# Optimization experiments

Hardware: AMD Instinct MI355X
Metric: run time of the kernel (lower is better)

## Reference

```python
import jax, jax.numpy as jnp
import numpy as np

N_NODES = 50000
N_EDGES = 1600000
IN_DIM = 128
HID = 128
SHARED = 64
N_GRAPHS = 2048


def setup_inputs() -> dict:
    key = jax.random.key(0)
    ks = jax.random.split(key, 16)
    x = jax.random.normal(ks[0], (N_NODES, IN_DIM), dtype=jnp.float32)
    edge_index = jax.random.randint(ks[1], (2, N_EDGES), 0, N_NODES, dtype=jnp.int64)
    batch = jnp.sort(jax.random.randint(ks[2], (N_NODES,), 0, N_GRAPHS, dtype=jnp.int64))

    def lin(k, fan_in, fan_out):
        bound = 1.0 / np.sqrt(fan_in)
        kw, kb = jax.random.split(k)
        W = jax.random.uniform(kw, (fan_in, fan_out), minval=-bound, maxval=bound, dtype=jnp.float32)
        b = jax.random.uniform(kb, (fan_out,), minval=-bound, maxval=bound, dtype=jnp.float32)
        return W, b

    W1a, b1a = lin(ks[3], IN_DIM, HID)
    W1b, b1b = lin(ks[4], HID, HID)
    W2a, b2a = lin(ks[5], HID, HID)
    W2b, b2b = lin(ks[6], HID, HID)
    Ws, bs = lin(ks[7], HID, SHARED)
    WlS, blS = lin(ks[8], SHARED, 1)
    WlP, blP = lin(ks[9], SHARED, 1)
    WnR, bnR = lin(ks[10], SHARED, 1)
    return dict(x=x, edge_index=edge_index, batch=batch,
                W1a=W1a, b1a=b1a, W1b=W1b, b1b=b1b,
                W2a=W2a, b2a=b2a, W2b=W2b, b2b=b2b,
                Ws=Ws, bs=bs, WlS=WlS, blS=blS, WlP=WlP, blP=blP, WnR=WnR, bnR=bnR)


def gin_conv(x, src, dst, Wa, ba, Wb, bb):
    # GINConv (eps=0): h_i = MLP(x_i + sum_{j->i} x_j)
    agg = jax.ops.segment_sum(x[src], dst, num_segments=N_NODES)
    h = x + agg
    h = jax.nn.relu(h @ Wa + ba)
    return h @ Wb + bb


def reference(x, edge_index, batch, W1a, b1a, W1b, b1b, W2a, b2a, W2b, b2b,
              Ws, bs, WlS, blS, WlP, blP, WnR, bnR):
    src, dst = edge_index[0], edge_index[1]
    h = jax.nn.relu(gin_conv(x, src, dst, W1a, b1a, W1b, b1b))
    h = jax.nn.relu(gin_conv(h, src, dst, W2a, b2a, W2b, b2b))
    # global mean pool over graph ids
    sums = jax.ops.segment_sum(h, batch, num_segments=N_GRAPHS)
    counts = jax.ops.segment_sum(jnp.ones((h.shape[0],), h.dtype), batch, num_segments=N_GRAPHS)
    pooled = sums / jnp.maximum(counts, 1.0)[:, None]
    g = jax.nn.relu(pooled @ Ws + bs)
    out_logS = (g @ WlS + blS)[:, 0]
    out_logP = (g @ WlP + blP)[:, 0]
    out_NR = (g @ WnR + bnR)[:, 0]
    return (out_logS, out_logP, out_NR)
```

## Files before the change

### kernel.cpp

```cpp
#include <hip/hip_runtime.h>
#include <hip/hip_bf16.h>


#define IN_DIM 128
#define NFINE 128
#define BIN_EPB 4096
#define SRCCH 8

typedef float  f32x4  __attribute__((ext_vector_type(4)));
typedef short  bf16x4 __attribute__((ext_vector_type(4)));
typedef short  bf16x8 __attribute__((ext_vector_type(8)));

__device__ __forceinline__ unsigned short bf16_rne(float v) {
    unsigned u = __float_as_uint(v);
    unsigned t = u + 0x7fffu + ((u >> 16) & 1u);
    return (unsigned short)(t >> 16);
}


__global__ __launch_bounds__(256) void f32_to_bf16_kernel(
    const float4* __restrict__ in, uint4* __restrict__ out, int n8)
{
    int i = blockIdx.x * 256 + threadIdx.x;
    if (i >= n8) return;
    float4 a = in[i * 2];
    float4 b = in[i * 2 + 1];
    float v[8] = {a.x, a.y, a.z, a.w, b.x, b.y, b.z, b.w};
    unsigned r[4];
#pragma unroll
    for (int j = 0; j < 4; ++j)
        r[j] = (unsigned)bf16_rne(v[j * 2]) | ((unsigned)bf16_rne(v[j * 2 + 1]) << 16);
    out[i] = make_uint4(r[0], r[1], r[2], r[3]);
}


__global__ __launch_bounds__(256) void conv_weights_kernel(
    const float* __restrict__ W0, const float* __restrict__ W1,
    const float* __restrict__ W2, const float* __restrict__ W3,
    unsigned short* __restrict__ Wh, unsigned short* __restrict__ Wl)
{
    int m   = blockIdx.x >> 6;
    int idx = (blockIdx.x & 63) * 256 + threadIdx.x;
    const float* W = (m == 0) ? W0 : (m == 1) ? W1 : (m == 2) ? W2 : W3;
    int k = idx >> 7, n = idx & 127;
    float v = W[idx];
    unsigned short hh = bf16_rne(v);
    float hf = __uint_as_float(((unsigned)hh) << 16);
    unsigned short ll = bf16_rne(v - hf);
    Wh[m * 16384 + n * 128 + k] = hh;
    Wl[m * 16384 + n * 128 + k] = ll;
}


__global__ __launch_bounds__(256) void bin_kernel(
    const int* __restrict__ src, const int* __restrict__ dst,
    int2* __restrict__ buckets, int* __restrict__ bcur,
    int n_edges, int n_nodes, int cap)
{
    __shared__ int cnt[NFINE];
    __shared__ int base[NFINE];
    for (int i = threadIdx.x; i < NFINE; i += 256) cnt[i] = 0;
    __syncthreads();

    const int e0 = blockIdx.x * BIN_EPB + threadIdx.x * 16;
    int ne = n_edges - e0;
    if (ne < 0) ne = 0;
    if (ne > 16) ne = 16;

    int d[16], s[16], off[16];
    if (ne == 16) {
#pragma unroll
        for (int q = 0; q < 4; ++q) {
            int4 dv = *(const int4*)(dst + e0 + q * 4);
            int4 sv = *(const int4*)(src + e0 + q * 4);
            d[q * 4 + 0] = dv.x; d[q * 4 + 1] = dv.y;
            d[q * 4 + 2] = dv.z; d[q * 4 + 3] = dv.w;
            s[q * 4 + 0] = sv.x; s[q * 4 + 1] = sv.y;
            s[q * 4 + 2] = sv.z; s[q * 4 + 3] = sv.w;
        }
    } else {
#pragma unroll
        for (int j = 0; j < 16; ++j) {
            d[j] = (j < ne) ? dst[e0 + j] : 0;
            s[j] = (j < ne) ? src[e0 + j] : 0;
        }
    }
#pragma unroll
    for (int j = 0; j < 16; ++j)
        if (j < ne) {
            int b = (int)(((long long)d[j] * NFINE) / n_nodes);
            off[j] = atomicAdd(&cnt[b], 1);
        }
    __syncthreads();
    for (int i = threadIdx.x; i < NFINE; i += 256)
        base[i] = atomicAdd(&bcur[i], cnt[i]);
    __syncthreads();
#pragma unroll
    for (int j = 0; j < 16; ++j)
        if (j < ne) {
            int b = (int)(((long long)d[j] * NFINE) / n_nodes);
            buckets[(size_t)b * cap + base[b] + off[j]] = make_int2(d[j], s[j]);
        }
}

__global__ __launch_bounds__(512) void csr_fused_kernel(
    const int2* __restrict__ buckets, const int* __restrict__ bcnt,
    int* __restrict__ row_start, int* __restrict__ csr_src,
    int cap, int n_nodes, int n_edges)
{
    __shared__ int bc[NFINE];
    __shared__ int h[4096];
    __shared__ int tsum[512];
    __shared__ int bbase_s;

    const int b = blockIdx.x;
    const int t = threadIdx.x;
    const int lo_n = (int)(((long long)b * n_nodes + NFINE - 1) / NFINE);
    const int hi_n = (int)(((long long)(b + 1) * n_nodes + NFINE - 1) / NFINE);
    const int sl = hi_n - lo_n;

    if (t < NFINE) bc[t] = bcnt[t];
#pragma unroll
    for (int j = 0; j < 8; ++j) h[t * 8 + j] = 0;
    __syncthreads();
    if (t == 0) {
        int s = 0;
        for (int i = 0; i < b; ++i) s += bc[i];
        bbase_s = s;
    }
    const int nb = bc[b];
    const int2* bp = buckets + (size_t)b * cap;
    __syncthreads();

    for (int i = t; i < nb; i += 512) {
        int2 e = bp[i];
        int key = (e.x - lo_n) * SRCCH + (int)(((long long)e.y * SRCCH) / n_nodes);
        atomicAdd(&h[key], 1);
    }
    __syncthreads();

    int base = 0;
#pragma unroll
    for (int j = 0; j < 8; ++j) {
        int v = h[t * 8 + j];
        h[t * 8 + j] = base;
        base += v;
    }
    tsum[t] = base;
    __syncthreads();
    int incl = tsum[t];
    for (int off = 1; off < 512; off <<= 1) {
        int tmp = (t >= off) ? tsum[t - off] : 0;
        __syncthreads();
        tsum[t] += tmp;
        __syncthreads();
        incl = tsum[t];
    }
    int texcl = incl - base + bbase_s;
#pragma unroll
    for (int j = 0; j < 8; ++j) h[t * 8 + j] += texcl;
    if (t < sl) row_start[lo_n + t] = h[t * SRCCH];
    if (b == NFINE - 1 && t == 0) row_start[n_nodes] = n_edges;
    __syncthreads();

    for (int i = t; i < nb; i += 512) {
        int2 e = bp[i];
        int key = (e.x - lo_n) * SRCCH + (int)(((long long)e.y * SRCCH) / n_nodes);
        csr_src[atomicAdd(&h[key], 1)] = e.y;
    }
}


__device__ __forceinline__ void add_row8(float acc[8], uint4 r) {
    union { unsigned u; float f; } c;
    c.u = r.x << 16;         acc[0] += c.f;
    c.u = r.x & 0xffff0000u; acc[1] += c.f;
    c.u = r.y << 16;         acc[2] += c.f;
    c.u = r.y & 0xffff0000u; acc[3] += c.f;
    c.u = r.z << 16;         acc[4] += c.f;
    c.u = r.z & 0xffff0000u; acc[5] += c.f;
    c.u = r.w << 16;         acc[6] += c.f;
    c.u = r.w & 0xffff0000u; acc[7] += c.f;
}

__global__ __launch_bounds__(256) void gather_agg_bf16_kernel(
    const float* __restrict__ xf,
    const uint4* __restrict__ xb,
    const int* __restrict__ row_start, const int* __restrict__ csr_src,
    float* __restrict__ out, int n_nodes)
{
    int t = blockIdx.x * 256 + threadIdx.x;
    int node = t >> 4;
    int lane = t & 15;
    if (node >= n_nodes) return;
    int lo = row_start[node];
    int hi = row_start[node + 1];

    const f32x4* xfr = (const f32x4*)(xf + (size_t)node * IN_DIM + lane * 8);
    f32x4 a0 = __builtin_nontemporal_load(xfr);
    f32x4 a1 = __builtin_nontemporal_load(xfr + 1);
    float acc[8] = {a0.x, a0.y, a0.z, a0.w, a1.x, a1.y, a1.z, a1.w};

    int e = lo;
    for (; e + 3 < hi; e += 4) {
        int s0 = csr_src[e];
        int s1 = csr_src[e + 1];
        int s2 = csr_src[e + 2];
        int s3 = csr_src[e + 3];
        uint4 r0 = xb[(size_t)s0 * 16 + lane];
        uint4 r1 = xb[(size_t)s1 * 16 + lane];
        uint4 r2 = xb[(size_t)s2 * 16 + lane];
        uint4 r3 = xb[(size_t)s3 * 16 + lane];
        add_row8(acc, r0);
        add_row8(acc, r1);
        add_row8(acc, r2);
        add_row8(acc, r3);
    }
    for (; e < hi; ++e) {
        uint4 r = xb[(size_t)csr_src[e] * 16 + lane];
        add_row8(acc, r);
    }

    f32x4 o0 = {acc[0], acc[1], acc[2], acc[3]};
    f32x4 o1 = {acc[4], acc[5], acc[6], acc[7]};
    f32x4* op = (f32x4*)(out + (size_t)node * IN_DIM + lane * 8);
    __builtin_nontemporal_store(o0, op);
    __builtin_nontemporal_store(o1, op + 1);
}

#define HSTRIDE 132

template <bool EMIT_BF16>
__global__ __launch_bounds__(128) void fused_mlp_kernel(
    const float* __restrict__ A,
    const unsigned short* __restrict__ Wa_h, const unsigned short* __restrict__ Wa_l,
    const float* __restrict__ ba,
    const unsigned short* __restrict__ Wb_h, const unsigned short* __restrict__ Wb_l,
    const float* __restrict__ bb,
    float* __restrict__ C, unsigned short* __restrict__ Cb, int M)
{
    __shared__ __align__(16) unsigned short Hh[64][HSTRIDE];
    __shared__ __align__(16) unsigned short Hl[64][HSTRIDE];

    const int t    = threadIdx.x;
    const int wave = t >> 6;
    const int lane = t & 63;
    const int l15  = lane & 15;
    const int quad = lane >> 4;
    const int wrow0 = wave * 32;
    const int row0  = blockIdx.x * 64 + wrow0;

    f32x4 acc[2][8];
#pragma unroll
    for (int ti = 0; ti < 2; ++ti)
#pragma unroll
        for (int ct = 0; ct < 8; ++ct) acc[ti][ct] = {0.f, 0.f, 0.f, 0.f};

    {
        int ar0 = row0 + l15;
        int ar1 = row0 + 16 + l15;
        const float* ap0 = A + (size_t)((ar0 < M) ? ar0 : (M - 1)) * IN_DIM + quad * 8;
        const float* ap1 = A + (size_t)((ar1 < M) ? ar1 : (M - 1)) * IN_DIM + quad * 8;
#pragma unroll
        for (int k0 = 0; k0 < IN_DIM; k0 += 32) {
            bf16x8 ah[2], al[2];
#pragma unroll
            for (int ti = 0; ti < 2; ++ti) {
                const float* ap = ti ? ap1 : ap0;
                f32x4 v0 = *(const f32x4*)(ap + k0);
                f32x4 v1 = *(const f32x4*)(ap + k0 + 4);
                float v[8] = {v0.x, v0.y, v0.z, v0.w, v1.x, v1.y, v1.z, v1.w};
                unsigned short h[8], l[8];
#pragma unroll
                for (int j = 0; j < 8; ++j) {
                    unsigned short hh = bf16_rne(v[j]);
                    h[j] = hh;
                    l[j] = bf16_rne(v[j] - __uint_as_float(((unsigned)hh) << 16));
                }
                ah[ti] = *(const bf16x8*)h;
                al[ti] = *(const bf16x8*)l;
            }
#pragma unroll
            for (int ct = 0; ct < 8; ++ct) {
                const size_t woff = (size_t)(ct * 16 + l15) * IN_DIM + k0 + quad * 8;
                bf16x8 wh = *(const bf16x8*)(Wa_h + woff);
                bf16x8 wl = *(const bf16x8*)(Wa_l + woff);
                acc[0][ct] = __builtin_amdgcn_mfma_f32_16x16x32_bf16(ah[0], wh, acc[0][ct], 0, 0, 0);
                acc[1][ct] = __builtin_amdgcn_mfma_f32_16x16x32_bf16(ah[1], wh, acc[1][ct], 0, 0, 0);
                acc[0][ct] = __builtin_amdgcn_mfma_f32_16x16x32_bf16(al[0], wh, acc[0][ct], 0, 0, 0);
                acc[1][ct] = __builtin_amdgcn_mfma_f32_16x16x32_bf16(al[1], wh, acc[1][ct], 0, 0, 0);
                acc[0][ct] = __builtin_amdgcn_mfma_f32_16x16x32_bf16(ah[0], wl, acc[0][ct], 0, 0, 0);
                acc[1][ct] = __builtin_amdgcn_mfma_f32_16x16x32_bf16(ah[1], wl, acc[1][ct], 0, 0, 0);
            }
        }
    }

#pragma unroll
    for (int ti = 0; ti < 2; ++ti) {
#pragma unroll
        for (int ct = 0; ct < 8; ++ct) {
            int col = ct * 16 + l15;
            float b = ba[col];
#pragma unroll
            for (int r = 0; r < 4; ++r) {
                int rl = wrow0 + ti * 16 + quad * 4 + r;
                float v = fmaxf(acc[ti][ct][r] + b, 0.f);
                unsigned short hh = bf16_rne(v);
                Hh[rl][col] = hh;
                Hl[rl][col] = bf16_rne(v - __uint_as_float(((unsigned)hh) << 16));
            }
            acc[ti][ct] = {0.f, 0.f, 0.f, 0.f};
        }
    }
    __syncthreads();

#pragma unroll
    for (int k0 = 0; k0 < IN_DIM; k0 += 32) {
        const int hk = k0 + quad * 8;
        bf16x8 ah[2], al[2];
#pragma unroll
        for (int ti = 0; ti < 2; ++ti) {
            const int hr = wrow0 + ti * 16 + l15;
            bf16x4 h0 = *(const bf16x4*)&Hh[hr][hk];
            bf16x4 h1 = *(const bf16x4*)&Hh[hr][hk + 4];
            bf16x4 l0 = *(const bf16x4*)&Hl[hr][hk];
            bf16x4 l1 = *(const bf16x4*)&Hl[hr][hk + 4];
            ah[ti] = __builtin_shufflevector(h0, h1, 0, 1, 2, 3, 4, 5, 6, 7);
            al[ti] = __builtin_shufflevector(l0, l1, 0, 1, 2, 3, 4, 5, 6, 7);
        }
#pragma unroll
        for (int ct = 0; ct < 8; ++ct) {
            const size_t woff = (size_t)(ct * 16 + l15) * IN_DIM + k0 + quad * 8;
            bf16x8 wh = *(const bf16x8*)(Wb_h + woff);
            bf16x8 wl = *(const bf16x8*)(Wb_l + woff);
            acc[0][ct] = __builtin_amdgcn_mfma_f32_16x16x32_bf16(ah[0], wh, acc[0][ct], 0, 0, 0);
            acc[1][ct] = __builtin_amdgcn_mfma_f32_16x16x32_bf16(ah[1], wh, acc[1][ct], 0, 0, 0);
            acc[0][ct] = __builtin_amdgcn_mfma_f32_16x16x32_bf16(al[0], wh, acc[0][ct], 0, 0, 0);
            acc[1][ct] = __builtin_amdgcn_mfma_f32_16x16x32_bf16(al[1], wh, acc[1][ct], 0, 0, 0);
            acc[0][ct] = __builtin_amdgcn_mfma_f32_16x16x32_bf16(ah[0], wl, acc[0][ct], 0, 0, 0);
            acc[1][ct] = __builtin_amdgcn_mfma_f32_16x16x32_bf16(ah[1], wl, acc[1][ct], 0, 0, 0);
        }
    }

#pragma unroll
    for (int ti = 0; ti < 2; ++ti) {
        const int rbase = row0 + ti * 16 + quad * 4;
#pragma unroll
        for (int ct = 0; ct < 8; ++ct) {
            int col = ct * 16 + l15;
            float b = bb[col];
#pragma unroll
            for (int r = 0; r < 4; ++r) {
                int row = rbase + r;
                if (row < M) {
                    float o = fmaxf(acc[ti][ct][r] + b, 0.f);
                    C[(size_t)row * IN_DIM + col] = o;
                    if (EMIT_BF16)
                        Cb[(size_t)row * IN_DIM + col] = bf16_rne(o);
                }
            }
        }
    }
}


__device__ __forceinline__ int lower_bound_i(const int* __restrict__ a, int n, int v) {
    int lo = 0, hi = n;
    while (lo < hi) {
        int mid = (lo + hi) >> 1;
        if (a[mid] < v) lo = mid + 1; else hi = mid;
    }
    return lo;
}

__global__ __launch_bounds__(128) void pool_kernel(
    const float* __restrict__ h, const int* __restrict__ batch,
    float* __restrict__ pooled, int n_nodes, int n_graphs)
{
    int g = blockIdx.x;
    int lo = lower_bound_i(batch, n_nodes, g);
    int hi = lower_bound_i(batch, n_nodes, g + 1);
    int j = threadIdx.x;
    float acc = 0.f;
    for (int i = lo; i < hi; ++i)
        acc += h[(size_t)i * IN_DIM + j];
    float cnt = (float)(hi - lo);
    pooled[(size_t)g * IN_DIM + j] = acc / fmaxf(cnt, 1.0f);
}

__global__ __launch_bounds__(64) void head_kernel(
    const float* __restrict__ pooled,
    const float* __restrict__ Ws,  const float* __restrict__ bs,
    const float* __restrict__ WlS, const float* __restrict__ blS,
    const float* __restrict__ WlP, const float* __restrict__ blP,
    const float* __restrict__ WnR, const float* __restrict__ bnR,
    float* __restrict__ out, int n_graphs)
{
    int g = blockIdx.x;
    int j = threadIdx.x;
    const float* p = pooled + (size_t)g * IN_DIM;
    float acc = bs[j];
#pragma unroll 8
    for (int k = 0; k < IN_DIM; ++k)
        acc = fmaf(p[k], Ws[k * 64 + j], acc);
    float gj = fmaxf(acc, 0.f);
    float s1 = gj * WlS[j];
    float s2 = gj * WlP[j];
    float s3 = gj * WnR[j];
#pragma unroll
    for (int off = 32; off > 0; off >>= 1) {
        s1 += __shfl_down(s1, off);
        s2 += __shfl_down(s2, off);
        s3 += __shfl_down(s3, off);
    }
    if (j == 0) {
        out[g]                = s1 + blS[0];
        out[n_graphs + g]     = s2 + blP[0];
        out[2 * n_graphs + g] = s3 + bnR[0];
    }
}


extern "C" void kernel_launch(void* const* d_in, const int* in_sizes, int n_in,
                              void* d_out, int out_size, void* d_ws, size_t ws_size,
                              hipStream_t stream)
{
    const float* x   = (const float*)d_in[0];
    const int*   ei  = (const int*)d_in[1];
    const int*   bat = (const int*)d_in[2];
    const float* W1a = (const float*)d_in[3];
    const float* b1a = (const float*)d_in[4];
    const float* W1b = (const float*)d_in[5];
    const float* b1b = (const float*)d_in[6];
    const float* W2a = (const float*)d_in[7];
    const float* b2a = (const float*)d_in[8];
    const float* W2b = (const float*)d_in[9];
    const float* b2b = (const float*)d_in[10];
    const float* Ws  = (const float*)d_in[11];
    const float* bs  = (const float*)d_in[12];
    const float* WlS = (const float*)d_in[13];
    const float* blS = (const float*)d_in[14];
    const float* WlP = (const float*)d_in[15];
    const float* blP = (const float*)d_in[16];
    const float* WnR = (const float*)d_in[17];
    const float* bnR = (const float*)d_in[18];

    const int n_nodes  = in_sizes[0] / IN_DIM;
    const int n_edges  = in_sizes[1] / 2;
    const int n_graphs = out_size / 3;
    const int* src = ei;
    const int* dst = ei + n_edges;

    const size_t node_elems   = (size_t)n_nodes * IN_DIM;
    const size_t pooled_elems = (size_t)n_graphs * IN_DIM;

    float* xbf    = (float*)d_ws;
    float* buf2   = xbf  + node_elems;
    float* bufA   = buf2 + node_elems;
    float* pooled = bufA + node_elems;
    int* row_start = (int*)(pooled + pooled_elems);
    int* bcur      = row_start + (n_nodes + 1);
    int* csr_src   = bcur + NFINE;
    unsigned short* wt_h = (unsigned short*)(csr_src + n_edges);
    unsigned short* wt_l = wt_h + 4 * 16384;

    unsigned short* xb = (unsigned short*)xbf;
    const int cap = n_edges / NFINE + 2048;
    int2* buckets = (int2*)bufA;

    const int gatherblocks = (int)(((size_t)n_nodes * 16 + 255) / 256);
    const int mlpblocks = (n_nodes + 63) / 64;
    const int binblocks = (n_edges + BIN_EPB - 1) / BIN_EPB;
    const int n8 = (int)(node_elems / 8);
    const int cvtblocks = (n8 + 255) / 256;

    conv_weights_kernel<<<256, 256, 0, stream>>>(W1a, W1b, W2a, W2b, wt_h, wt_l);
    hipMemsetAsync(bcur, 0, NFINE * sizeof(int), stream);
    bin_kernel<<<binblocks, 256, 0, stream>>>(src, dst, buckets, bcur,
                                              n_edges, n_nodes, cap);
    csr_fused_kernel<<<NFINE, 512, 0, stream>>>(buckets, bcur, row_start,
                                                csr_src, cap, n_nodes, n_edges);

    f32_to_bf16_kernel<<<cvtblocks, 256, 0, stream>>>((const float4*)x, (uint4*)xb, n8);
    gather_agg_bf16_kernel<<<gatherblocks, 256, 0, stream>>>(
        x, (const uint4*)xb, row_start, csr_src, bufA, n_nodes);
    fused_mlp_kernel<true><<<mlpblocks, 128, 0, stream>>>(
        bufA, wt_h, wt_l, b1a, wt_h + 16384, wt_l + 16384, b1b,
        buf2, xb, n_nodes);

    gather_agg_bf16_kernel<<<gatherblocks, 256, 0, stream>>>(
        buf2, (const uint4*)xb, row_start, csr_src, bufA, n_nodes);
    fused_mlp_kernel<false><<<mlpblocks, 128, 0, stream>>>(
        bufA, wt_h + 2 * 16384, wt_l + 2 * 16384, b2a,
        wt_h + 3 * 16384, wt_l + 3 * 16384, b2b,
        buf2, nullptr, n_nodes);

    pool_kernel<<<n_graphs, 128, 0, stream>>>(buf2, bat, pooled, n_nodes, n_graphs);
    head_kernel<<<n_graphs, 64, 0, stream>>>(pooled, Ws, bs, WlS, blS, WlP, blP,
                                             WnR, bnR, (float*)d_out, n_graphs);
}
```

Before: 376.2 us.

## Split MLP output columns across four waves and refine CSR source chunking

The fused MLP kernel now runs 256 threads per block. Each wave handles 32 rows and 64 output columns instead of 32 rows and all 128 columns, which halves the accumulators per thread and doubles the waves per tile. The goal is higher occupancy and less register pressure. Separately, CSR construction sorts edges within each destination node into 16 source-range chunks instead of 8, using a larger shared histogram, to improve locality of the later source-row gathers. The cost is more shared memory and scan work in the CSR kernel, and each A tile is now converted and loaded by two waves instead of one.

```diff
diff --git a/kernel.cpp b/kernel.cpp
--- a/kernel.cpp
+++ b/kernel.cpp
@@ -5,7 +5,9 @@
 #define IN_DIM 128
 #define NFINE 128
 #define BIN_EPB 4096
-#define SRCCH 8
+#define SRCCH 16
+#define NSLOT 6400
+#define SPT 13
 
 typedef float  f32x4  __attribute__((ext_vector_type(4)));
 typedef short  bf16x4 __attribute__((ext_vector_type(4)));
@@ -109,7 +111,7 @@
     int cap, int n_nodes, int n_edges)
 {
     __shared__ int bc[NFINE];
-    __shared__ int h[4096];
+    __shared__ int h[NSLOT];
     __shared__ int tsum[512];
     __shared__ int bbase_s;
 
@@ -120,8 +122,7 @@
     const int sl = hi_n - lo_n;
 
     if (t < NFINE) bc[t] = bcnt[t];
-#pragma unroll
-    for (int j = 0; j < 8; ++j) h[t * 8 + j] = 0;
+    for (int i = t; i < NSLOT; i += 512) h[i] = 0;
     __syncthreads();
     if (t == 0) {
         int s = 0;
@@ -141,10 +142,13 @@
 
     int base = 0;
 #pragma unroll
-    for (int j = 0; j < 8; ++j) {
-        int v = h[t * 8 + j];
-        h[t * 8 + j] = base;
-        base += v;
+    for (int j = 0; j < SPT; ++j) {
+        int slot = t * SPT + j;
+        if (slot < NSLOT) {
+            int v = h[slot];
+            h[slot] = base;
+            base += v;
+        }
     }
     tsum[t] = base;
     __syncthreads();
@@ -158,8 +162,12 @@
     }
     int texcl = incl - base + bbase_s;
 #pragma unroll
-    for (int j = 0; j < 8; ++j) h[t * 8 + j] += texcl;
-    if (t < sl) row_start[lo_n + t] = h[t * SRCCH];
+    for (int j = 0; j < SPT; ++j) {
+        int slot = t * SPT + j;
+        if (slot < NSLOT) h[slot] += texcl;
+    }
+    __syncthreads();
+    for (int i = t; i < sl; i += 512) row_start[lo_n + i] = h[i * SRCCH];
     if (b == NFINE - 1 && t == 0) row_start[n_nodes] = n_edges;
     __syncthreads();
 
@@ -231,7 +239,7 @@
 #define HSTRIDE 132
 
 template <bool EMIT_BF16>
-__global__ __launch_bounds__(128) void fused_mlp_kernel(
+__global__ __launch_bounds__(256) void fused_mlp_kernel(
     const float* __restrict__ A,
     const unsigned short* __restrict__ Wa_h, const unsigned short* __restrict__ Wa_l,
     const float* __restrict__ ba,
@@ -247,14 +255,15 @@
     const int lane = t & 63;
     const int l15  = lane & 15;
     const int quad = lane >> 4;
-    const int wrow0 = wave * 32;
-    const int row0  = blockIdx.x * 64 + wrow0;
-
-    f32x4 acc[2][8];
+    const int rw   = (wave & 1) * 32;
+    const int cw   = (wave >> 1) * 64;
+    const int row0 = blockIdx.x * 64 + rw;
+
+    f32x4 acc[2][4];
 #pragma unroll
     for (int ti = 0; ti < 2; ++ti)
 #pragma unroll
-        for (int ct = 0; ct < 8; ++ct) acc[ti][ct] = {0.f, 0.f, 0.f, 0.f};
+        for (int ct = 0; ct < 4; ++ct) acc[ti][ct] = {0.f, 0.f, 0.f, 0.f};
 
     {
         int ar0 = row0 + l15;
@@ -281,8 +290,8 @@
                 al[ti] = *(const bf16x8*)l;
             }
 #pragma unroll
-            for (int ct = 0; ct < 8; ++ct) {
-                const size_t woff = (size_t)(ct * 16 + l15) * IN_DIM + k0 + quad * 8;
+            for (int ct = 0; ct < 4; ++ct) {
+                const size_t woff = (size_t)(cw + ct * 16 + l15) * IN_DIM + k0 + quad * 8;
                 bf16x8 wh = *(const bf16x8*)(Wa_h + woff);
                 bf16x8 wl = *(const bf16x8*)(Wa_l + woff);
                 acc[0][ct] = __builtin_amdgcn_mfma_f32_16x16x32_bf16(ah[0], wh, acc[0][ct], 0, 0, 0);
@@ -298,12 +307,12 @@
 #pragma unroll
     for (int ti = 0; ti < 2; ++ti) {
 #pragma unroll
-        for (int ct = 0; ct < 8; ++ct) {
-            int col = ct * 16 + l15;
+        for (int ct = 0; ct < 4; ++ct) {
+            int col = cw + ct * 16 + l15;
             float b = ba[col];
 #pragma unroll
             for (int r = 0; r < 4; ++r) {
-                int rl = wrow0 + ti * 16 + quad * 4 + r;
+                int rl = rw + ti * 16 + quad * 4 + r;
                 float v = fmaxf(acc[ti][ct][r] + b, 0.f);
                 unsigned short hh = bf16_rne(v);
                 Hh[rl][col] = hh;
@@ -320,7 +329,7 @@
         bf16x8 ah[2], al[2];
 #pragma unroll
         for (int ti = 0; ti < 2; ++ti) {
-            const int hr = wrow0 + ti * 16 + l15;
+            const int hr = rw + ti * 16 + l15;
             bf16x4 h0 = *(const bf16x4*)&Hh[hr][hk];
             bf16x4 h1 = *(const bf16x4*)&Hh[hr][hk + 4];
             bf16x4 l0 = *(const bf16x4*)&Hl[hr][hk];
@@ -329,8 +338,8 @@
             al[ti] = __builtin_shufflevector(l0, l1, 0, 1, 2, 3, 4, 5, 6, 7);
         }
 #pragma unroll
-        for (int ct = 0; ct < 8; ++ct) {
-            const size_t woff = (size_t)(ct * 16 + l15) * IN_DIM + k0 + quad * 8;
+        for (int ct = 0; ct < 4; ++ct) {
+            const size_t woff = (size_t)(cw + ct * 16 + l15) * IN_DIM + k0 + quad * 8;
             bf16x8 wh = *(const bf16x8*)(Wb_h + woff);
             bf16x8 wl = *(const bf16x8*)(Wb_l + woff);
             acc[0][ct] = __builtin_amdgcn_mfma_f32_16x16x32_bf16(ah[0], wh, acc[0][ct], 0, 0, 0);
@@ -346,8 +355,8 @@
     for (int ti = 0; ti < 2; ++ti) {
         const int rbase = row0 + ti * 16 + quad * 4;
 #pragma unroll
-        for (int ct = 0; ct < 8; ++ct) {
-            int col = ct * 16 + l15;
+        for (int ct = 0; ct < 4; ++ct) {
+            int col = cw + ct * 16 + l15;
             float b = bb[col];
 #pragma unroll
             for (int r = 0; r < 4; ++r) {
@@ -484,13 +493,13 @@
     f32_to_bf16_kernel<<<cvtblocks, 256, 0, stream>>>((const float4*)x, (uint4*)xb, n8);
     gather_agg_bf16_kernel<<<gatherblocks, 256, 0, stream>>>(
         x, (const uint4*)xb, row_start, csr_src, bufA, n_nodes);
-    fused_mlp_kernel<true><<<mlpblocks, 128, 0, stream>>>(
+    fused_mlp_kernel<true><<<mlpblocks, 256, 0, stream>>>(
         bufA, wt_h, wt_l, b1a, wt_h + 16384, wt_l + 16384, b1b,
         buf2, xb, n_nodes);
 
     gather_agg_bf16_kernel<<<gatherblocks, 256, 0, stream>>>(
         buf2, (const uint4*)xb, row_start, csr_src, bufA, n_nodes);
-    fused_mlp_kernel<false><<<mlpblocks, 128, 0, stream>>>(
+    fused_mlp_kernel<false><<<mlpblocks, 256, 0, stream>>>(
         bufA, wt_h + 2 * 16384, wt_l + 2 * 16384, b2a,
         wt_h + 3 * 16384, wt_l + 3 * 16384, b2b,
         buf2, nullptr, n_nodes);
```

Result: no change. 372.9 us (-0.9%).
